# Performance work log

Hardware: AMD Instinct MI355X
Metric: run time of the kernel (lower is better)

The kernel has to match this reference:

```python
import jax, jax.numpy as jnp
import numpy as np

BN_EPS = 1e-5


def conv1d(x, w, pad):
    # x: [N, Cin, L], w: [Cout, Cin, K] -> [N, Cout, L]
    return jax.lax.conv_general_dilated(
        x, w, window_strides=(1,), padding=[(pad, pad)],
        dimension_numbers=("NCH", "OIH", "NCH"))


def setup_inputs() -> dict:
    key = jax.random.key(0)
    k1, k2, k3, k4 = jax.random.split(key, 4)
    b, c, h, w = 32, 512, 64, 64
    x = jax.random.normal(k1, (b, c, h, w), jnp.float32)
    # ECA-style channel conv: kernel_size=5 for channel=512
    w1 = jax.random.normal(k2, (1, 1, 5), jnp.float32) * 0.3
    # Spatial convs created in forward: Conv1d(h,h,3) and Conv1d(w,w,3)
    wh = jax.random.normal(k3, (h, h, 3), jnp.float32) * (1.0 / np.sqrt(3.0 * h))
    ww = jax.random.normal(k4, (w, w, 3), jnp.float32) * (1.0 / np.sqrt(3.0 * w))
    gamma = jnp.ones((1,), jnp.float32)
    beta = jnp.zeros((1,), jnp.float32)
    return {"x": x, "w1": w1, "wh": wh, "ww": ww, "gamma": gamma, "beta": beta}


def reference(x, w1, wh, ww, gamma, beta):
    b, c, h, w = x.shape
    # Channel attention: global avg pool -> conv1d over channel axis -> sigmoid
    f1 = jnp.mean(x, axis=(2, 3)).reshape(b, 1, c)          # [b,1,c]
    f1 = conv1d(f1, w1, pad=2).reshape(b, c, 1, 1)
    f1 = jax.nn.sigmoid(f1)
    F = x * f1
    # Spatial attention: channel-mean -> conv1d along w (channels=h) + conv1d along h (channels=w)
    f2 = jnp.mean(x, axis=1)                                 # [b,h,w]
    f2_h = conv1d(f2, wh, pad=1).reshape(b, 1, h, w)
    f2_w = conv1d(jnp.transpose(f2, (0, 2, 1)), ww, pad=1)   # [b,w,h]
    f2_w = jnp.transpose(f2_w, (0, 2, 1)).reshape(b, 1, h, w)
    f2 = f2_h + f2_w
    # BatchNorm2d(1), training-mode batch statistics over (b, h, w)
    mu = jnp.mean(f2)
    var = jnp.mean(jnp.square(f2 - mu))
    f2 = gamma[0] * (f2 - mu) * jax.lax.rsqrt(var + BN_EPS) + beta[0]
    return F * jax.nn.sigmoid(f2)
```

## Files before the change

kernel.cpp:

```cpp
#include <hip/hip_runtime.h>

#define NB 32
#define NC 512
#define NH 64
#define NW 64
#define NHW 4096
#define NTOT ((size_t)NB * NC * NHW)

typedef float f32x4 __attribute__((ext_vector_type(4)));

#define OFF_S1PART 0
#define OFF_F2PART 262144
#define OFF_F1SIG  1310720
#define OFF_F2RAW  1327104
#define OFF_BNPART 1458176

__global__ __launch_bounds__(256) void k_reduce(const float* __restrict__ x,
                                                float* __restrict__ s1part,
                                                float* __restrict__ f2part) {
  __shared__ f32x4 comb[4][64];
  const int bid = blockIdx.x;
  const int jc = bid & 15;
  const int cg = (bid >> 4) & 7;
  const int b = bid >> 7;
  const int tid = threadIdx.x;
  const int lane = tid & 63;
  const int wv = tid >> 6;

  const size_t base =
      ((size_t)(b * NC + cg * 64 + wv * 16)) * NHW + jc * 256 + lane * 4;
  f32x4 p = {0.f, 0.f, 0.f, 0.f};
  float myS = 0.f;
#pragma unroll
  for (int k = 0; k < 16; ++k) {
    const f32x4 v = *reinterpret_cast<const f32x4*>(x + base + (size_t)k * NHW);
    p += v;
    float s = (v.x + v.y) + (v.z + v.w);
#pragma unroll
    for (int m = 32; m > 0; m >>= 1) s += __shfl_xor(s, m);
    myS = (lane == k) ? s : myS;
  }
  if (lane < 16)
    s1part[(size_t)(b * NC + cg * 64 + wv * 16 + lane) * 16 + jc] = myS;

  comb[wv][lane] = p;
  __syncthreads();
  if (tid < 64) {
    const f32x4 r =
        (comb[0][tid] + comb[1][tid]) + (comb[2][tid] + comb[3][tid]);
    reinterpret_cast<f32x4*>(f2part)[((size_t)cg * NB + b) * 1024 + jc * 64 +
                                     tid] = r;
  }
}

__global__ __launch_bounds__(256) void k_f2(const float* __restrict__ f2part,
                                            const float* __restrict__ s1part,
                                            const float* __restrict__ w1,
                                            const float* __restrict__ wh,
                                            const float* __restrict__ ww,
                                            float* __restrict__ f2raw,
                                            float* __restrict__ bnpart,
                                            float* __restrict__ f1sig) {
  __shared__ float mp[66][66];
  __shared__ float wwL[64][193];
  __shared__ float red[8];
  const int b = blockIdx.x >> 4;
  const int rg = blockIdx.x & 15;
  const int tid = threadIdx.x;

  if (tid < 66) {
    mp[0][tid] = 0.f;
    mp[65][tid] = 0.f;
    mp[tid][0] = 0.f;
    mp[tid][65] = 0.f;
  }
  for (int t = tid; t < 64 * 192; t += 256) wwL[t / 192][t % 192] = ww[t];
#pragma unroll
  for (int t4 = tid; t4 < 1024; t4 += 256) {
    f32x4 s = {0.f, 0.f, 0.f, 0.f};
#pragma unroll
    for (int cg = 0; cg < 8; ++cg)
      s += reinterpret_cast<const f32x4*>(f2part +
                                          ((size_t)(cg * NB + b)) * NHW)[t4];
    s *= (1.0f / (float)NC);
    const int r = t4 >> 4;
    const int c = (t4 & 15) * 4;
    mp[1 + r][1 + c + 0] = s.x;
    mp[1 + r][1 + c + 1] = s.y;
    mp[1 + r][1 + c + 2] = s.z;
    mp[1 + r][1 + c + 3] = s.w;
  }
  __syncthreads();

  const int i = rg * 4 + (tid >> 6);
  const int j = tid & 63;
  const float* whp = wh + 192 * __builtin_amdgcn_readfirstlane(i);
  const float* wwp = &wwL[j][0];
  float acc = 0.f;
#pragma unroll 16
  for (int ic = 0; ic < 64; ++ic) {
    acc += whp[ic * 3 + 0] * mp[ic + 1][j] +
           whp[ic * 3 + 1] * mp[ic + 1][j + 1] +
           whp[ic * 3 + 2] * mp[ic + 1][j + 2];
    acc += wwp[ic * 3 + 0] * mp[i][ic + 1] +
           wwp[ic * 3 + 1] * mp[i + 1][ic + 1] +
           wwp[ic * 3 + 2] * mp[i + 2][ic + 1];
  }
  f2raw[(size_t)b * NHW + (i << 6) + j] = acc;

  float lsum = acc, lsq = acc * acc;
#pragma unroll
  for (int off = 32; off > 0; off >>= 1) {
    lsum += __shfl_down(lsum, off);
    lsq += __shfl_down(lsq, off);
  }
  if ((tid & 63) == 0) {
    red[(tid >> 6) * 2 + 0] = lsum;
    red[(tid >> 6) * 2 + 1] = lsq;
  }
  __syncthreads();
  if (tid == 0) {
    bnpart[blockIdx.x * 2 + 0] = red[0] + red[2] + red[4] + red[6];
    bnpart[blockIdx.x * 2 + 1] = red[1] + red[3] + red[5] + red[7];
  }

  if (rg == 0) {
#pragma unroll
    for (int c0 = 0; c0 < 512; c0 += 256) {
      const int c = c0 + tid;
      float acc5 = 0.f;
#pragma unroll
      for (int k = 0; k < 5; ++k) {
        const int cc = c + k - 2;
        if (cc >= 0 && cc < NC) {
          const f32x4* sp =
              reinterpret_cast<const f32x4*>(s1part + (size_t)(b * NC + cc) * 16);
          const f32x4 a = (sp[0] + sp[1]) + (sp[2] + sp[3]);
          acc5 += w1[k] * ((a.x + a.y) + (a.z + a.w));
        }
      }
      acc5 *= (1.0f / (float)NHW);
      f1sig[b * NC + c] = 1.0f / (1.0f + __expf(-acc5));
    }
  }
}

__global__ __launch_bounds__(256) void k_out(const float* __restrict__ x,
                                             const float* __restrict__ f1sig,
                                             const float* __restrict__ f2raw,
                                             const float* __restrict__ bnpart,
                                             const float* __restrict__ gamma,
                                             const float* __restrict__ beta,
                                             float* __restrict__ out) {
  __shared__ float bnv[2];
  const int tid = threadIdx.x;
  if (tid < 64) {
    float s = 0.f, q = 0.f;
#pragma unroll
    for (int r = 0; r < 8; ++r) {
      s += bnpart[2 * (tid + 64 * r) + 0];
      q += bnpart[2 * (tid + 64 * r) + 1];
    }
#pragma unroll
    for (int off = 32; off > 0; off >>= 1) {
      s += __shfl_down(s, off);
      q += __shfl_down(q, off);
    }
    if (tid == 0) {
      const float N = (float)(NB * NHW);
      const float mu = s / N;
      const float var = q / N - mu * mu;
      bnv[0] = mu;
      bnv[1] = gamma[0] * rsqrtf(var + 1e-5f);
    }
  }
  __syncthreads();
  const float mu = bnv[0];
  const float g = bnv[1];
  const float bt = beta[0];

  const int bid = gridDim.x - 1 - blockIdx.x;
  const int gid = bid * 256 + tid;
  const int hw4 = gid & 1023;
  const int cq = gid >> 10;
  const f32x4* xp = reinterpret_cast<const f32x4*>(x) + gid;
  const f32x4* fp = reinterpret_cast<const f32x4*>(f2raw) + hw4;
  const float* f1p = f1sig + cq;
  f32x4* op = reinterpret_cast<f32x4*>(out) + gid;

  for (int b = NB - 1; b >= 0; --b) {
    const f32x4 xv = xp[(size_t)b * 524288];
    const f32x4 fv = fp[(size_t)b * 1024];
    const float f1 = f1p[(size_t)b * 512];
    f32x4 ov;
    ov.x = xv.x * f1 * (1.0f / (1.0f + __expf(-(g * (fv.x - mu) + bt))));
    ov.y = xv.y * f1 * (1.0f / (1.0f + __expf(-(g * (fv.y - mu) + bt))));
    ov.z = xv.z * f1 * (1.0f / (1.0f + __expf(-(g * (fv.z - mu) + bt))));
    ov.w = xv.w * f1 * (1.0f / (1.0f + __expf(-(g * (fv.w - mu) + bt))));
    __builtin_nontemporal_store(ov, op + (size_t)b * 524288);
  }
}

extern "C" void kernel_launch(void* const* d_in, const int* in_sizes, int n_in,
                              void* d_out, int out_size, void* d_ws,
                              size_t ws_size, hipStream_t stream) {
  const float* x = (const float*)d_in[0];
  const float* w1 = (const float*)d_in[1];
  const float* wh = (const float*)d_in[2];
  const float* ww = (const float*)d_in[3];
  const float* gamma = (const float*)d_in[4];
  const float* beta = (const float*)d_in[5];
  float* out = (float*)d_out;
  float* ws = (float*)d_ws;

  float* s1part = ws + OFF_S1PART;
  float* f2part = ws + OFF_F2PART;
  float* f1sig = ws + OFF_F1SIG;
  float* f2raw = ws + OFF_F2RAW;
  float* bnpart = ws + OFF_BNPART;

  k_reduce<<<NB * 8 * 16, 256, 0, stream>>>(x, s1part, f2part);
  k_f2<<<NB * 16, 256, 0, stream>>>(f2part, s1part, w1, wh, ww, f2raw, bnpart,
                                    f1sig);
  k_out<<<2048, 256, 0, stream>>>(x, f1sig, f2raw, bnpart, gamma, beta, out);
}
```

Before: 159.1 us.

## Remap output kernel to reduce-kernel tiling, reuse spatial sigmoid across channels

The output kernel now uses the same block decomposition as the reduction kernel (batch, channel group, spatial chunk) with 4096 blocks. Each thread computes the spatial sigmoid once for its four pixels and reuses it across 16 channels, instead of recomputing it per element. Block order is reversed in groups of 8, so the tail of x, which the reduction kernel touched most recently, is read first and may still be in L2/MALL. The trade-off is a different memory access pattern and more blocks, each doing less work.

After: 146.8 us. 1.08x faster.

```diff
diff --git a/kernel.cpp b/kernel.cpp
--- a/kernel.cpp
+++ b/kernel.cpp
@@ -179,25 +179,34 @@
   const float g = bnv[1];
   const float bt = beta[0];
 
-  const int bid = gridDim.x - 1 - blockIdx.x;
-  const int gid = bid * 256 + tid;
-  const int hw4 = gid & 1023;
-  const int cq = gid >> 10;
-  const f32x4* xp = reinterpret_cast<const f32x4*>(x) + gid;
-  const f32x4* fp = reinterpret_cast<const f32x4*>(f2raw) + hw4;
-  const float* f1p = f1sig + cq;
-  f32x4* op = reinterpret_cast<f32x4*>(out) + gid;
-
-  for (int b = NB - 1; b >= 0; --b) {
-    const f32x4 xv = xp[(size_t)b * 524288];
-    const f32x4 fv = fp[(size_t)b * 1024];
-    const float f1 = f1p[(size_t)b * 512];
-    f32x4 ov;
-    ov.x = xv.x * f1 * (1.0f / (1.0f + __expf(-(g * (fv.x - mu) + bt))));
-    ov.y = xv.y * f1 * (1.0f / (1.0f + __expf(-(g * (fv.y - mu) + bt))));
-    ov.z = xv.z * f1 * (1.0f / (1.0f + __expf(-(g * (fv.z - mu) + bt))));
-    ov.w = xv.w * f1 * (1.0f / (1.0f + __expf(-(g * (fv.w - mu) + bt))));
-    __builtin_nontemporal_store(ov, op + (size_t)b * 524288);
+  const int grp = blockIdx.x >> 3;
+  const int bid = (511 - grp) * 8 + (blockIdx.x & 7);
+  const int jc = bid & 15;
+  const int cg = (bid >> 4) & 7;
+  const int b = bid >> 7;
+  const int lane = tid & 63;
+  const int wv = tid >> 6;
+
+  const int px = jc * 256 + lane * 4;
+  const f32x4 fv = *reinterpret_cast<const f32x4*>(f2raw + b * NHW + px);
+  f32x4 s2;
+  s2.x = 1.0f / (1.0f + __expf(-(g * (fv.x - mu) + bt)));
+  s2.y = 1.0f / (1.0f + __expf(-(g * (fv.y - mu) + bt)));
+  s2.z = 1.0f / (1.0f + __expf(-(g * (fv.z - mu) + bt)));
+  s2.w = 1.0f / (1.0f + __expf(-(g * (fv.w - mu) + bt)));
+
+  const int cbase = __builtin_amdgcn_readfirstlane(b * NC + cg * 64 + wv * 16);
+  float f1v[16];
+#pragma unroll
+  for (int k = 0; k < 16; ++k) f1v[k] = f1sig[cbase + k];
+
+  const size_t base = (size_t)cbase * NHW + px;
+#pragma unroll
+  for (int k = 0; k < 16; ++k) {
+    const f32x4 xv = *reinterpret_cast<const f32x4*>(x + base + (size_t)k * NHW);
+    const f32x4 ov = xv * (s2 * f1v[k]);
+    __builtin_nontemporal_store(
+        ov, reinterpret_cast<f32x4*>(out + base + (size_t)k * NHW));
   }
 }
 
@@ -222,5 +231,6 @@
   k_reduce<<<NB * 8 * 16, 256, 0, stream>>>(x, s1part, f2part);
   k_f2<<<NB * 16, 256, 0, stream>>>(f2part, s1part, w1, wh, ww, f2raw, bnpart,
                                     f1sig);
-  k_out<<<2048, 256, 0, stream>>>(x, f1sig, f2raw, bnpart, gamma, beta, out);
-}
+  k_out<<<NB * 8 * 16, 256, 0, stream>>>(x, f1sig, f2raw, bnpart, gamma, beta,
+                                         out);
+}
```
